# Performance work log

Hardware: AMD Instinct MI355X
Metric: run time of the kernel (lower is better)

Reference implementation:

```python
import jax, jax.numpy as jnp
import numpy as np

B, S, P, H, W, TAG, M, K = 4, 2, 17, 128, 128, 1, 8, 10
PHW = P * H * W
SIGMA, SF = 0.2, 3.0
E_INV = float(np.e ** -1)
EPS = 1e-6


def setup_inputs() -> dict:
    key = jax.random.key(0)
    k1, k2, k3, k4, k5, k6, k7 = jax.random.split(key, 7)
    preds = jax.random.normal(k1, (B, S, (1 + TAG) * P, H, W), jnp.float32)
    gt_masks = jax.random.uniform(k2, (B, H, W), jnp.float32)
    gt_heatmaps = jax.random.uniform(k3, (B, P, H, W), jnp.float32)
    pos = jax.random.uniform(k4, (B, M, P, 2), jnp.float32) * H  # pixel coords
    vis = jax.random.randint(k5, (B, M, P, 1), 0, 2).astype(jnp.float32)
    gt_skeletons = jnp.concatenate([pos, vis], axis=-1)  # [B,M,P,3] = (x, y, vis)
    kp_idx = jax.random.randint(k6, (B, M, P, 1), 0, PHW)
    kp_vis = jax.random.randint(k7, (B, M, P, 1), 0, 2)
    gt_keypoints = jnp.concatenate([kp_idx, kp_vis], axis=-1).astype(jnp.int32)  # [B,M,J,2]
    return {"preds": preds, "gt_masks": gt_masks, "gt_heatmaps": gt_heatmaps,
            "gt_skeletons": gt_skeletons, "gt_keypoints": gt_keypoints}


def _clog(x):
    # torch BCE clamps log at -100
    return jnp.clip(jnp.log(x), -100.0, None)


def _tag_single(pt, kp):
    # pt: [TAG, PHW] tag map for one (image, stack); kp: [M, J, 2] int (flat_idx, vis)
    idx = kp[..., 0]
    vis = (kp[..., 1] > 0).astype(pt.dtype)  # [M, J]
    g = jnp.transpose(pt[:, idx], (1, 2, 0))  # [M, J, TAG]
    cnt = vis.sum(1)  # [M]
    valid = (cnt > 0).astype(pt.dtype)
    safe = jnp.maximum(cnt, 1.0)
    mean_tag = (g * vis[..., None]).sum(1) / safe[:, None]  # [M, TAG]
    # pull: per-person mean over (visible joints x tag dims) of squared deviation
    pull_pp = (((g - mean_tag[:, None]) ** 2) * vis[..., None]).sum((1, 2)) / (safe * TAG)
    num = valid.sum()
    pull = (pull_pp * valid).sum() / (num + EPS)
    d = ((mean_tag[:, None] - mean_tag[None]) ** 2).sum(-1)  # [M, M]
    pm = jnp.exp(-d) * valid[:, None] * valid[None]
    push = (pm.sum() - num) / ((num - 1.0) * num + EPS) * 0.5
    return push, pull


def _forward(preds, gt_masks, gt_heatmaps, gt_skeletons, gt_keypoints):
    hm = preds[:, :, :P]  # [B,S,P,H,W] raw heatmap logits
    prob = jax.nn.sigmoid(hm)
    # ---- detection loss (weighted BCE, per stack) ----
    t = (gt_heatmaps > E_INV).astype(jnp.float32)[:, None]  # [B,1,P,H,W]
    wgt = 10.0 * t + 0.5 * (gt_heatmaps < E_INV).astype(jnp.float32)[:, None]
    x = prob * gt_masks[:, None, None]
    bce = -(t * _clog(x) + (1.0 - t) * _clog(1.0 - x))
    det_loss = (wgt * bce).mean(axis=(0, 2, 3, 4))  # [S]
    # ---- associative embedding push/pull ----
    pred_tag_imgs = preds[:, :, P:(1 + TAG) * P].reshape(B, S, TAG, P, H, W)
    pred_tags = pred_tag_imgs.reshape(B, S, TAG, PHW)
    push, pull = jax.vmap(lambda ptb, kpb: jax.vmap(lambda pt: _tag_single(pt, kpb))(ptb))(
        pred_tags, gt_keypoints)  # each [B,S]
    # ---- keypoint sampling: top-K of flattened probability maps ----
    flat = prob.reshape(B, S, PHW)
    _, topi = jax.lax.top_k(flat, K)  # [B,S,K]
    part = topi // (H * W)
    rem = topi % (H * W)
    xi = rem // W
    yi = rem % W
    pos = jnp.stack([xi, yi], -1).astype(jnp.float32)  # [B,S,K,2]
    # ---- nearest-person matching (faithful to source, incl. vis==1 penalty) ----
    max_dist = float(H + W)
    sk_t = jnp.transpose(gt_skeletons, (0, 2, 1, 3))  # [B,P,M,3]
    pidx = jnp.broadcast_to(part.reshape(B, S * K)[:, :, None, None], (B, S * K, M, 3))
    sk_sel = jnp.take_along_axis(sk_t, pidx, axis=1).reshape(B, S, K, M, 3)
    vispen = max_dist * (sk_sel[..., 2] == 1).astype(jnp.float32)  # [B,S,K,M]
    dvec = vispen[..., None] + sk_sel[..., 1:] - pos[..., None, :]
    dist = jnp.sqrt((dvec ** 2).sum(-1) + 1e-12)
    person_ids = jnp.argmin(dist, axis=-1)  # [B,S,K]
    # ---- gather tag values at sampled locations ----
    pti = jnp.transpose(pred_tag_imgs, (0, 1, 3, 4, 5, 2))  # [B,S,P,H,W,TAG]
    bb = jnp.arange(B)[:, None, None]
    ss = jnp.arange(S)[None, :, None]
    tv = pti[bb, ss, part, xi, yi]  # [B,S,K,TAG]
    # ---- SkeletonGenerator: tag-conditioned soft-argmax ----
    aff = ((pti[:, :, None] - tv[:, :, :, None, None, None, :]) ** 2).sum(-1)  # [B,S,K,P,H,W]
    logits = SF * hm[:, :, None] - aff / (2.0 * SIGMA ** 2)
    wts = jax.nn.softmax(logits.reshape(B, S, K, P, H * W), -1).reshape(B, S, K, P, H, W)
    px = (wts * jnp.arange(H, dtype=jnp.float32)[:, None]).sum((-1, -2))  # [B,S,K,P]
    py = (wts * jnp.arange(W, dtype=jnp.float32)).sum((-1, -2))
    skel = jnp.stack([px, py], -1)  # [B,S,K,P,2]
    gts = gt_skeletons[bb, person_ids]  # [B,S,K,P,3]
    err = jnp.sqrt(((gts[..., :2] - skel) ** 2).sum(-1) + 1e-12) * (gts[..., 2] > 0)
    delta = 0.1
    a = jnp.abs(err)
    small = (a < delta).astype(jnp.float32)
    hub = small * err ** 2 + (1.0 - small) * delta * (a - delta / 2.0)
    skel_loss = hub.mean(-1).mean(-1)  # [B,S]
    # ---- weighted sum (loss_weights = (1,1,1,10)) ----
    return (1.0 * push.mean() + 1.0 * pull.mean() + 1.0 * det_loss.mean()
            + 10.0 * skel_loss.mean())


def reference(preds, gt_masks, gt_heatmaps, gt_skeletons, gt_keypoints):
    return _forward(preds, gt_masks, gt_heatmaps, gt_skeletons, gt_keypoints)
```

## Files before the change

kernel.cpp:

```cpp
#include <hip/hip_runtime.h>
#include <math.h>

#define B_ 4
#define S_ 2
#define P_ 17
#define H_ 128
#define W_ 128
#define M_ 8
#define K_ 10
#define HW_ (H_*W_)
#define PHW_ (P_*HW_)
#define CH_ 34
#define G_ 34
#define C_ (PHW_/G_)
#define E_INV_F 0.36787944117144233f
#define LOG2E 1.4426950408889634f
#define SF_ 3.0f
#define INV2SIG 12.5f
#define MAXDIST 256.0f

#define TOP1_BLOCKS (B_*S_*G_)
#define DET_BLOCKS  544
#define TAG_BLOCKS  (B_*S_)
#define MAIN_BLOCKS (TOP1_BLOCKS + DET_BLOCKS + TAG_BLOCKS)

__device__ __forceinline__ unsigned int map32(float f) {
    unsigned int u = __float_as_uint(f);
    unsigned int flip = (unsigned int)((int)u >> 31) | 0x80000000u;
    return u ^ flip;
}

__device__ __forceinline__ void insert10(unsigned long long* a, unsigned long long key) {
    #pragma unroll
    for (int j = 9; j >= 1; --j) {
        unsigned long long am1 = a[j-1];
        a[j] = (key > am1) ? am1 : ((key > a[j]) ? key : a[j]);
    }
    a[0] = (key > a[0]) ? key : a[0];
}

__device__ __forceinline__ void merge10(unsigned long long* a, const unsigned long long* b) {
    #pragma unroll
    for (int t = 0; t < 10; ++t) {
        unsigned long long key = b[t];
        if (key > a[9]) insert10(a, key);
    }
}

__global__ __launch_bounds__(256) void k_main(const float* __restrict__ preds,
                                              const float* __restrict__ gmask,
                                              const float* __restrict__ gh,
                                              const int* __restrict__ kp,
                                              unsigned long long* __restrict__ cand,
                                              float* __restrict__ out) {
    int tid = threadIdx.x;
    if (blockIdx.x < TOP1_BLOCKS) {
        int bs = blockIdx.x / G_;
        int c  = blockIdx.x % G_;
        int wave = tid >> 6, lane = tid & 63;
        const float4* base = (const float4*)(preds + (size_t)bs*CH_*HW_ + (size_t)c*C_);
        unsigned long long a[10];
        #pragma unroll
        for (int j = 0; j < 10; ++j) a[j] = 0ull;
        for (int j = 0; j < 8; ++j) {
            int idx4 = wave*512 + j*64 + lane;
            float4 v = base[idx4];
            unsigned int i0 = (unsigned int)(c*C_ + idx4*4);
            const float* vv = &v.x;
            #pragma unroll
            for (int cc = 0; cc < 4; ++cc) {
                unsigned int key32 = map32(vv[cc]);
                unsigned int thr = (unsigned int)(a[9] >> 32);
                unsigned long long mask = __ballot(key32 >= thr);
                if (mask) {
                    unsigned long long kk =
                        ((unsigned long long)key32 << 32) | (unsigned int)(~(i0 + cc));
                    do {
                        int l = (int)__ffsll(mask) - 1;
                        unsigned long long cnd = __shfl(kk, l);
                        if (cnd > a[9]) insert10(a, cnd);
                        mask &= mask - 1;
                    } while (mask);
                }
            }
        }
        __shared__ unsigned long long smw[4][10];
        if (lane == 0) {
            #pragma unroll
            for (int j = 0; j < 10; ++j) smw[wave][j] = a[j];
        }
        __syncthreads();
        if (tid < 2) {
            unsigned long long x[10], y[10];
            #pragma unroll
            for (int j = 0; j < 10; ++j) { x[j] = smw[tid][j]; y[j] = smw[tid+2][j]; }
            merge10(x, y);
            #pragma unroll
            for (int j = 0; j < 10; ++j) smw[tid][j] = x[j];
        }
        __syncthreads();
        if (tid == 0) {
            unsigned long long x[10], y[10];
            #pragma unroll
            for (int j = 0; j < 10; ++j) { x[j] = smw[0][j]; y[j] = smw[1][j]; }
            merge10(x, y);
            #pragma unroll
            for (int j = 0; j < 10; ++j) cand[(size_t)blockIdx.x*10 + j] = x[j];
        }
    } else if (blockIdx.x < TOP1_BLOCKS + DET_BLOCKS) {
        int t = (blockIdx.x - TOP1_BLOCKS)*256 + tid;
        float acc = 0.0f;
        #pragma unroll
        for (int j = 0; j < 4; ++j) {
            int q = t + j*(DET_BLOCKS*256);
            int hw4 = q & 4095;
            int t1  = q >> 12;
            int p   = t1 % P_;
            int t2  = t1 / P_;
            float4 hm4 = ((const float4*)preds)[(t2*CH_ + p)*4096 + hw4];
            float4 gm4 = ((const float4*)gmask)[(t2>>1)*4096 + hw4];
            float4 gh4 = ((const float4*)gh)[((t2>>1)*P_ + p)*4096 + hw4];
            const float* hmv = &hm4.x; const float* gmv = &gm4.x; const float* ghv4 = &gh4.x;
            #pragma unroll
            for (int cc = 0; cc < 4; ++cc) {
                float hm = hmv[cc];
                float e = exp2f(-fabsf(hm)*LOG2E);
                float r = __builtin_amdgcn_rcpf(1.0f + e);
                float prob = (hm >= 0.0f) ? r : e*r;
                float x = prob * gmv[cc];
                float ghv = ghv4[cc];
                float tt  = (ghv > E_INV_F) ? 1.0f : 0.0f;
                float wgt = 10.0f*tt + ((ghv < E_INV_F) ? 0.5f : 0.0f);
                float lx  = fmaxf(__logf(x),        -100.0f);
                float l1x = fmaxf(__logf(1.0f - x), -100.0f);
                acc += wgt * (-(tt*lx + (1.0f - tt)*l1x));
            }
        }
        #pragma unroll
        for (int off = 32; off > 0; off >>= 1) acc += __shfl_down(acc, off);
        __shared__ float sred[4];
        int wave = tid >> 6, lane = tid & 63;
        if (lane == 0) sred[wave] = acc;
        __syncthreads();
        if (tid == 0) {
            float sum = sred[0] + sred[1] + sred[2] + sred[3];
            atomicAdd(out, sum * (1.0f/(float)(B_*S_*P_*HW_)));
        }
    } else {
        int bs = blockIdx.x - (TOP1_BLOCKS + DET_BLOCKS);
        int b = bs / S_;
        __shared__ float g[M_*P_];
        __shared__ float vis[M_*P_];
        __shared__ float mean_tag[M_];
        __shared__ float validm[M_];
        __shared__ float pull_pp[M_];
        const float* tagbase = preds + ((size_t)bs*CH_ + P_)*HW_;
        if (tid < M_*P_) {
            int m = tid / P_; int p = tid % P_;
            int off = ((b*M_ + m)*P_ + p)*2;
            int idx = kp[off];
            int v   = kp[off+1];
            g[tid]   = tagbase[idx];
            vis[tid] = (v > 0) ? 1.0f : 0.0f;
        }
        __syncthreads();
        if (tid < M_) {
            float cnt = 0.0f, sum = 0.0f;
            for (int p = 0; p < P_; p++) { cnt += vis[tid*P_+p]; sum += g[tid*P_+p]*vis[tid*P_+p]; }
            float safe = fmaxf(cnt, 1.0f);
            float mt = sum / safe;
            mean_tag[tid] = mt;
            validm[tid] = (cnt > 0.0f) ? 1.0f : 0.0f;
            float pp = 0.0f;
            for (int p = 0; p < P_; p++) { float d = g[tid*P_+p] - mt; pp += d*d*vis[tid*P_+p]; }
            pull_pp[tid] = pp / safe;
        }
        __syncthreads();
        if (tid == 0) {
            float num = 0.0f;
            for (int m = 0; m < M_; m++) num += validm[m];
            float pull = 0.0f;
            for (int m = 0; m < M_; m++) pull += pull_pp[m]*validm[m];
            pull = pull / (num + 1e-6f);
            float pmsum = 0.0f;
            for (int i = 0; i < M_; i++)
                for (int j = 0; j < M_; j++) {
                    float d = mean_tag[i] - mean_tag[j]; d = d*d;
                    pmsum += expf(-d)*validm[i]*validm[j];
                }
            float push = (pmsum - num) / ((num - 1.0f)*num + 1e-6f) * 0.5f;
            atomicAdd(out, (push + pull) * (1.0f/(float)(B_*S_)));
        }
    }
}

__global__ __launch_bounds__(64) void k_top2(const float* __restrict__ preds,
                                             const float* __restrict__ gsk,
                                             const unsigned long long* __restrict__ cand,
                                             float* __restrict__ ws_tv,
                                             int* __restrict__ ws_pid) {
    int bs = blockIdx.x; int b = bs / S_;
    int tid = threadIdx.x;
    __shared__ unsigned long long sm[64*10];
    if (tid < G_) {
        #pragma unroll
        for (int j = 0; j < 10; ++j) sm[tid*10+j] = cand[((size_t)bs*G_ + tid)*10 + j];
    } else {
        #pragma unroll
        for (int j = 0; j < 10; ++j) sm[tid*10+j] = 0ull;
    }
    __syncthreads();
    for (int st = 32; st >= 1; st >>= 1) {
        if (tid < st) {
            unsigned long long x[10], y[10];
            #pragma unroll
            for (int j = 0; j < 10; ++j) { x[j] = sm[tid*10+j]; y[j] = sm[(tid+st)*10+j]; }
            merge10(x, y);
            #pragma unroll
            for (int j = 0; j < 10; ++j) sm[tid*10+j] = x[j];
        }
        __syncthreads();
    }
    if (tid < K_) {
        unsigned long long key = sm[tid];
        unsigned int topi = (unsigned int)(~key);
        int part = topi >> 14;
        int rem  = topi & (HW_-1);
        int xi   = rem >> 7;
        int yi   = rem & (W_-1);
        const float* tagbase = preds + ((size_t)bs*CH_ + P_)*HW_;
        float tv = tagbase[topi];
        float best = INFINITY; int pid = 0;
        for (int m = 0; m < M_; m++) {
            const float* sk = gsk + ((size_t)(b*M_ + m)*P_ + part)*3;
            float sk1 = sk[1], sk2 = sk[2];
            float vp = (sk2 == 1.0f) ? MAXDIST : 0.0f;
            float d0 = vp + sk1 - (float)xi;
            float d1 = vp + sk2 - (float)yi;
            float dist = sqrtf(d0*d0 + d1*d1 + 1e-12f);
            if (dist < best) { best = dist; pid = m; }
        }
        int o = bs*K_ + tid;
        ws_tv[o]  = tv;
        ws_pid[o] = pid;
    }
}

__global__ __launch_bounds__(1024) void k_skel(const float* __restrict__ preds,
                                               const float* __restrict__ gsk,
                                               const float* __restrict__ ws_tv,
                                               const int* __restrict__ ws_pid,
                                               float* __restrict__ out) {
    int bid = blockIdx.x;
    int p  = bid % P_;
    int bs = bid / P_;
    int b  = bs / S_;
    const float4* hm4 = (const float4*)(preds + ((size_t)bs*CH_ + p)*HW_);
    const float4* tg4 = (const float4*)(preds + ((size_t)bs*CH_ + P_ + p)*HW_);
    float tv[K_];
    #pragma unroll
    for (int k = 0; k < K_; k++) tv[k] = ws_tv[bs*K_ + k];
    float l[K_], sx[K_], sy[K_];
    #pragma unroll
    for (int k = 0; k < K_; k++) { l[k] = 0.0f; sx[k] = 0.0f; sy[k] = 0.0f; }
    int tid = threadIdx.x;
    const float C2 = INV2SIG * LOG2E;
    #pragma unroll
    for (int j = 0; j < HW_/4/1024; ++j) {
        int q = tid + j*1024;
        float4 hv = hm4[q];
        float4 tg = tg4[q];
        float h  = (float)(q >> 5);
        float w0 = (float)((q*4) & (W_-1));
        const float* hvv = &hv.x; const float* tgv = &tg.x;
        #pragma unroll
        for (int cc = 0; cc < 4; ++cc) {
            float a2 = (SF_*LOG2E) * hvv[cc];
            float tgc = tgv[cc];
            float w = w0 + (float)cc;
            #pragma unroll
            for (int k = 0; k < K_; k++) {
                float d = tgc - tv[k];
                float e = exp2f(fmaf(-C2, d*d, a2));
                l[k] += e;
                sx[k] = fmaf(e, h, sx[k]);
                sy[k] = fmaf(e, w, sy[k]);
            }
        }
    }
    #pragma unroll
    for (int k = 0; k < K_; k++) {
        for (int off = 32; off > 0; off >>= 1) {
            l[k]  += __shfl_down(l[k],  off);
            sx[k] += __shfl_down(sx[k], off);
            sy[k] += __shfl_down(sy[k], off);
        }
    }
    __shared__ float red[16][K_][3];
    int wave = tid >> 6, lane = tid & 63;
    if (lane == 0) {
        for (int k = 0; k < K_; k++) {
            red[wave][k][0] = l[k]; red[wave][k][1] = sx[k]; red[wave][k][2] = sy[k];
        }
    }
    __syncthreads();
    __shared__ float hubred[K_];
    if (tid < K_) {
        int k = tid;
        float L = 0.0f, SX = 0.0f, SY = 0.0f;
        #pragma unroll
        for (int w2 = 0; w2 < 16; w2++) {
            L += red[w2][k][0]; SX += red[w2][k][1]; SY += red[w2][k][2];
        }
        float px = SX / L, py = SY / L;
        int pid = ws_pid[bs*K_ + k];
        const float* g = gsk + ((size_t)(b*M_ + pid)*P_ + p)*3;
        float d0 = g[0] - px, d1 = g[1] - py;
        float gate = (g[2] > 0.0f) ? 1.0f : 0.0f;
        float err = sqrtf(d0*d0 + d1*d1 + 1e-12f) * gate;
        float hub = (err < 0.1f) ? err*err : 0.1f*(err - 0.05f);
        hubred[k] = hub;
    }
    __syncthreads();
    if (tid == 0) {
        float s = 0.0f;
        #pragma unroll
        for (int k = 0; k < K_; k++) s += hubred[k];
        atomicAdd(out, s * (10.0f/(float)(B_*S_*K_*P_)));
    }
}

extern "C" void kernel_launch(void* const* d_in, const int* in_sizes, int n_in,
                              void* d_out, int out_size, void* d_ws, size_t ws_size,
                              hipStream_t stream) {
    (void)in_sizes; (void)n_in; (void)out_size; (void)ws_size;
    const float* preds = (const float*)d_in[0];
    const float* gmask = (const float*)d_in[1];
    const float* gh    = (const float*)d_in[2];
    const float* gsk   = (const float*)d_in[3];
    const int*   gkp   = (const int*)d_in[4];
    float* out = (float*)d_out;
    unsigned long long* cand = (unsigned long long*)d_ws;
    float* ws_tv  = (float*)(cand + (size_t)B_*S_*G_*10);
    int*   ws_pid = (int*)(ws_tv + (size_t)B_*S_*K_);

    hipMemsetAsync(out, 0, sizeof(float), stream);
    hipLaunchKernelGGL(k_main, dim3(MAIN_BLOCKS), dim3(256), 0, stream,
                       preds, gmask, gh, gkp, cand, out);
    hipLaunchKernelGGL(k_top2, dim3(B_*S_),    dim3(64),   0, stream, preds, gsk, cand, ws_tv, ws_pid);
    hipLaunchKernelGGL(k_skel, dim3(B_*S_*P_), dim3(1024), 0, stream, preds, gsk, ws_tv, ws_pid, out);
}
```

Before: 160.3 us.

## Split skeleton softmax into chunked blocks and replace atomics with final reduction kernel

The skeleton kernel moves from 136 blocks of 1024 threads to 544 blocks of 256 threads, each handling a quarter of the H*W plane. It writes partial softmax sums to workspace. A new single-block finalize kernel combines the partials, computes the Huber loss and folds in the detection and tag partials that used to be atomically added. This removes the memset and the global atomics and spreads the skeleton work over more CUs, at the cost of an extra launch and a serial final kernel. Launch bounds hints are added.

```diff
diff --git a/kernel.cpp b/kernel.cpp
--- a/kernel.cpp
+++ b/kernel.cpp
@@ -24,6 +24,10 @@
 #define TAG_BLOCKS  (B_*S_)
 #define MAIN_BLOCKS (TOP1_BLOCKS + DET_BLOCKS + TAG_BLOCKS)
 
+#define SKEL_CHUNKS 4
+#define NBSP (B_*S_*P_)
+#define SKEL_BLOCKS (NBSP*SKEL_CHUNKS)
+
 __device__ __forceinline__ unsigned int map32(float f) {
     unsigned int u = __float_as_uint(f);
     unsigned int flip = (unsigned int)((int)u >> 31) | 0x80000000u;
@@ -47,12 +51,13 @@
     }
 }
 
-__global__ __launch_bounds__(256) void k_main(const float* __restrict__ preds,
-                                              const float* __restrict__ gmask,
-                                              const float* __restrict__ gh,
-                                              const int* __restrict__ kp,
-                                              unsigned long long* __restrict__ cand,
-                                              float* __restrict__ out) {
+__global__ __launch_bounds__(256, 4) void k_main(const float* __restrict__ preds,
+                                                 const float* __restrict__ gmask,
+                                                 const float* __restrict__ gh,
+                                                 const int* __restrict__ kp,
+                                                 unsigned long long* __restrict__ cand,
+                                                 float* __restrict__ ws_det,
+                                                 float* __restrict__ ws_tag) {
     int tid = threadIdx.x;
     if (blockIdx.x < TOP1_BLOCKS) {
         int bs = blockIdx.x / G_;
@@ -108,7 +113,8 @@
             for (int j = 0; j < 10; ++j) cand[(size_t)blockIdx.x*10 + j] = x[j];
         }
     } else if (blockIdx.x < TOP1_BLOCKS + DET_BLOCKS) {
-        int t = (blockIdx.x - TOP1_BLOCKS)*256 + tid;
+        int dblk = blockIdx.x - TOP1_BLOCKS;
+        int t = dblk*256 + tid;
         float acc = 0.0f;
         #pragma unroll
         for (int j = 0; j < 4; ++j) {
@@ -142,10 +148,7 @@
         int wave = tid >> 6, lane = tid & 63;
         if (lane == 0) sred[wave] = acc;
         __syncthreads();
-        if (tid == 0) {
-            float sum = sred[0] + sred[1] + sred[2] + sred[3];
-            atomicAdd(out, sum * (1.0f/(float)(B_*S_*P_*HW_)));
-        }
+        if (tid == 0) ws_det[dblk] = sred[0] + sred[1] + sred[2] + sred[3];
     } else {
         int bs = blockIdx.x - (TOP1_BLOCKS + DET_BLOCKS);
         int b = bs / S_;
@@ -189,7 +192,7 @@
                     pmsum += expf(-d)*validm[i]*validm[j];
                 }
             float push = (pmsum - num) / ((num - 1.0f)*num + 1e-6f) * 0.5f;
-            atomicAdd(out, (push + pull) * (1.0f/(float)(B_*S_)));
+            ws_tag[bs] = push + pull;
         }
     }
 }
@@ -246,15 +249,15 @@
     }
 }
 
-__global__ __launch_bounds__(1024) void k_skel(const float* __restrict__ preds,
-                                               const float* __restrict__ gsk,
-                                               const float* __restrict__ ws_tv,
-                                               const int* __restrict__ ws_pid,
-                                               float* __restrict__ out) {
-    int bid = blockIdx.x;
+__global__ __launch_bounds__(256, 4) void k_skel(const float* __restrict__ preds,
+                                                 const float* __restrict__ ws_tv,
+                                                 float* __restrict__ ws_skl,
+                                                 float* __restrict__ ws_ssx,
+                                                 float* __restrict__ ws_ssy) {
+    int bid   = blockIdx.x / SKEL_CHUNKS;
+    int chunk = blockIdx.x % SKEL_CHUNKS;
     int p  = bid % P_;
     int bs = bid / P_;
-    int b  = bs / S_;
     const float4* hm4 = (const float4*)(preds + ((size_t)bs*CH_ + p)*HW_);
     const float4* tg4 = (const float4*)(preds + ((size_t)bs*CH_ + P_ + p)*HW_);
     float tv[K_];
@@ -266,8 +269,8 @@
     int tid = threadIdx.x;
     const float C2 = INV2SIG * LOG2E;
     #pragma unroll
-    for (int j = 0; j < HW_/4/1024; ++j) {
-        int q = tid + j*1024;
+    for (int j = 0; j < 4; ++j) {
+        int q = chunk*1024 + j*256 + tid;
         float4 hv = hm4[q];
         float4 tg = tg4[q];
         float h  = (float)(q >> 5);
@@ -296,21 +299,49 @@
             sy[k] += __shfl_down(sy[k], off);
         }
     }
-    __shared__ float red[16][K_][3];
+    __shared__ float red[4][K_][3];
     int wave = tid >> 6, lane = tid & 63;
     if (lane == 0) {
+        #pragma unroll
         for (int k = 0; k < K_; k++) {
             red[wave][k][0] = l[k]; red[wave][k][1] = sx[k]; red[wave][k][2] = sy[k];
         }
     }
     __syncthreads();
-    __shared__ float hubred[K_];
     if (tid < K_) {
         int k = tid;
+        float L  = red[0][k][0] + red[1][k][0] + red[2][k][0] + red[3][k][0];
+        float SX = red[0][k][1] + red[1][k][1] + red[2][k][1] + red[3][k][1];
+        float SY = red[0][k][2] + red[1][k][2] + red[2][k][2] + red[3][k][2];
+        int o = blockIdx.x*K_ + k;
+        ws_skl[o] = L; ws_ssx[o] = SX; ws_ssy[o] = SY;
+    }
+}
+
+__global__ __launch_bounds__(256) void k_fin(const float* __restrict__ gsk,
+                                             const int* __restrict__ ws_pid,
+                                             const float* __restrict__ ws_skl,
+                                             const float* __restrict__ ws_ssx,
+                                             const float* __restrict__ ws_ssy,
+                                             const float* __restrict__ ws_det,
+                                             const float* __restrict__ ws_tag,
+                                             float* __restrict__ out) {
+    int tid = threadIdx.x;
+    float acc = 0.0f;
+    for (int i = tid; i < DET_BLOCKS; i += 256) acc += ws_det[i];
+    acc *= (1.0f/(float)(B_*S_*P_*HW_));
+    if (tid < B_*S_) acc += ws_tag[tid] * (1.0f/(float)(B_*S_));
+    for (int idx = tid; idx < NBSP*K_; idx += 256) {
+        int bid = idx / K_;
+        int k   = idx % K_;
+        int p  = bid % P_;
+        int bs = bid / P_;
+        int b  = bs / S_;
         float L = 0.0f, SX = 0.0f, SY = 0.0f;
         #pragma unroll
-        for (int w2 = 0; w2 < 16; w2++) {
-            L += red[w2][k][0]; SX += red[w2][k][1]; SY += red[w2][k][2];
+        for (int c = 0; c < SKEL_CHUNKS; ++c) {
+            int o = (bid*SKEL_CHUNKS + c)*K_ + k;
+            L += ws_skl[o]; SX += ws_ssx[o]; SY += ws_ssy[o];
         }
         float px = SX / L, py = SY / L;
         int pid = ws_pid[bs*K_ + k];
@@ -319,15 +350,15 @@
         float gate = (g[2] > 0.0f) ? 1.0f : 0.0f;
         float err = sqrtf(d0*d0 + d1*d1 + 1e-12f) * gate;
         float hub = (err < 0.1f) ? err*err : 0.1f*(err - 0.05f);
-        hubred[k] = hub;
-    }
+        acc += hub * (10.0f/(float)(B_*S_*K_*P_));
+    }
+    #pragma unroll
+    for (int off = 32; off > 0; off >>= 1) acc += __shfl_down(acc, off);
+    __shared__ float sred[4];
+    int wave = tid >> 6, lane = tid & 63;
+    if (lane == 0) sred[wave] = acc;
     __syncthreads();
-    if (tid == 0) {
-        float s = 0.0f;
-        #pragma unroll
-        for (int k = 0; k < K_; k++) s += hubred[k];
-        atomicAdd(out, s * (10.0f/(float)(B_*S_*K_*P_)));
-    }
+    if (tid == 0) out[0] = sred[0] + sred[1] + sred[2] + sred[3];
 }
 
 extern "C" void kernel_launch(void* const* d_in, const int* in_sizes, int n_in,
@@ -343,10 +374,18 @@
     unsigned long long* cand = (unsigned long long*)d_ws;
     float* ws_tv  = (float*)(cand + (size_t)B_*S_*G_*10);
     int*   ws_pid = (int*)(ws_tv + (size_t)B_*S_*K_);
-
-    hipMemsetAsync(out, 0, sizeof(float), stream);
+    float* ws_skl = (float*)(ws_pid + (size_t)B_*S_*K_);
+    float* ws_ssx = ws_skl + (size_t)SKEL_BLOCKS*K_;
+    float* ws_ssy = ws_ssx + (size_t)SKEL_BLOCKS*K_;
+    float* ws_det = ws_ssy + (size_t)SKEL_BLOCKS*K_;
+    float* ws_tag = ws_det + DET_BLOCKS;
+
     hipLaunchKernelGGL(k_main, dim3(MAIN_BLOCKS), dim3(256), 0, stream,
-                       preds, gmask, gh, gkp, cand, out);
-    hipLaunchKernelGGL(k_top2, dim3(B_*S_),    dim3(64),   0, stream, preds, gsk, cand, ws_tv, ws_pid);
-    hipLaunchKernelGGL(k_skel, dim3(B_*S_*P_), dim3(1024), 0, stream, preds, gsk, ws_tv, ws_pid, out);
-}
+                       preds, gmask, gh, gkp, cand, ws_det, ws_tag);
+    hipLaunchKernelGGL(k_top2, dim3(B_*S_),       dim3(64),  0, stream,
+                       preds, gsk, cand, ws_tv, ws_pid);
+    hipLaunchKernelGGL(k_skel, dim3(SKEL_BLOCKS), dim3(256), 0, stream,
+                       preds, ws_tv, ws_skl, ws_ssx, ws_ssy);
+    hipLaunchKernelGGL(k_fin,  dim3(1),           dim3(256), 0, stream,
+                       gsk, ws_pid, ws_skl, ws_ssx, ws_ssy, ws_det, ws_tag, out);
+}
```

New measurement: 130.2 us. 1.23x faster.
